# Optimization experiments

Measured on AMD Instinct MI355X. Metric: run time of the kernel, lower is better.

Reference implementation:

```python
import jax, jax.numpy as jnp
import numpy as np

B, S, D, DV = 1, 4096, 1024, 1024  # S == 4*D required by the data-dependent scale broadcast


def setup_inputs() -> dict:
    key = jax.random.key(0)
    kq, kk, kv, ks, kp = jax.random.split(key, 5)
    return {
        "q": jax.random.normal(kq, (B, S, D), dtype=jnp.float32),
        "k": jax.random.normal(kk, (B, S, D), dtype=jnp.float32),
        "v": jax.random.normal(kv, (B, S, DV), dtype=jnp.float32),
        "scale_factor": jax.random.normal(ks, (1,), dtype=jnp.float32),  # overwritten in forward
        "dropout_p": jax.random.uniform(kp, (1,), dtype=jnp.float32),   # overwritten in forward
    }


def reference(q, k, v, scale_factor, dropout_p):
    b, s, d = q.shape
    step = s // 4
    # data-dependent per-column scale: 4 strided rows of q flattened -> (B, 4*D) == (B, S)
    scale = q[:, ::step].reshape(b, -1)            # (B, S)
    qk = jnp.einsum('bsd,btd->bst', q, k)           # (B, S, S)
    scaled_qk = qk * scale[:, None, :]              # torch broadcast (B,S)->(1,1,S) since B==1
    softmax_qk = jax.nn.softmax(scaled_qk, axis=-1)
    # dropout with tensor p is ill-defined in torch; identity (eval semantics)
    return jnp.einsum('bst,btv->bsv', softmax_qk, v)
```

## Files before the change

kernel.cpp:

```cpp
#include <hip/hip_runtime.h>
#include <hip/hip_bf16.h>

typedef __bf16 bf16x8 __attribute__((ext_vector_type(8)));
typedef __bf16 bf16x4 __attribute__((ext_vector_type(4)));
typedef float f32x4 __attribute__((ext_vector_type(4)));

#define S_LEN 4096
#define DDIM  1024

#define MFMA __builtin_amdgcn_mfma_f32_16x16x32_bf16

#define BAR() do { asm volatile("" ::: "memory"); __builtin_amdgcn_s_barrier(); asm volatile("" ::: "memory"); } while (0)
#define VM6() asm volatile("s_waitcnt vmcnt(6)" ::: "memory")
#define VM4() asm volatile("s_waitcnt vmcnt(4)" ::: "memory")
#define VM0() asm volatile("s_waitcnt vmcnt(0)" ::: "memory")

__device__ __forceinline__ void gl_lds16(const __bf16* g, __bf16* l)
{
    __builtin_amdgcn_global_load_lds(
        (const __attribute__((address_space(1))) void*)g,
        (__attribute__((address_space(3))) void*)l, 16, 0, 0);
}

__global__ void prep_hilo(const float* __restrict__ q, const float* __restrict__ kk,
                          __bf16* __restrict__ qh, __bf16* __restrict__ ql,
                          __bf16* __restrict__ kh, __bf16* __restrict__ kl,
                          float* __restrict__ scale)
{
    const int gid = blockIdx.x * blockDim.x + threadIdx.x;
    if (gid < S_LEN) scale[gid] = q[((size_t)(gid >> 10) << 20) + (gid & 1023)];

    const int n8 = (S_LEN * DDIM) / 8;
    for (int i = gid; i < n8; i += gridDim.x * blockDim.x) {
        float4 a = *(const float4*)(q + (size_t)i * 8);
        float4 b = *(const float4*)(q + (size_t)i * 8 + 4);
        float va[8] = {a.x, a.y, a.z, a.w, b.x, b.y, b.z, b.w};
        bf16x8 h, l;
#pragma unroll
        for (int j = 0; j < 8; ++j) {
            __bf16 hh = (__bf16)va[j];
            h[j] = hh;
            l[j] = (__bf16)(va[j] - (float)hh);
        }
        *(bf16x8*)(qh + (size_t)i * 8) = h;
        *(bf16x8*)(ql + (size_t)i * 8) = l;

        a = *(const float4*)(kk + (size_t)i * 8);
        b = *(const float4*)(kk + (size_t)i * 8 + 4);
        float vb[8] = {a.x, a.y, a.z, a.w, b.x, b.y, b.z, b.w};
#pragma unroll
        for (int j = 0; j < 8; ++j) {
            __bf16 hh = (__bf16)vb[j];
            h[j] = hh;
            l[j] = (__bf16)(vb[j] - (float)hh);
        }
        *(bf16x8*)(kh + (size_t)i * 8) = h;
        *(bf16x8*)(kl + (size_t)i * 8) = l;
    }
}

__global__ void prep_vt(const float* __restrict__ v, __bf16* __restrict__ vt)
{
    __shared__ float tile[32][33];
    const int t0 = blockIdx.x * 32;
    const int d0 = blockIdx.y * 32;
    const int tx = threadIdx.x & 31;
    const int ty = threadIdx.x >> 5;
#pragma unroll
    for (int i = 0; i < 32; i += 8)
        tile[ty + i][tx] = v[(size_t)(t0 + ty + i) * DDIM + d0 + tx];
    __syncthreads();
#pragma unroll
    for (int i = 0; i < 32; i += 8)
        vt[(size_t)(d0 + ty + i) * S_LEN + t0 + tx] = (__bf16)tile[tx][ty + i];
}

__device__ __forceinline__ const __bf16* selA(const __bf16* qh, const __bf16* ql, int ps)
{ return ps == 1 ? ql : qh; }
__device__ __forceinline__ const __bf16* selB(const __bf16* kh, const __bf16* kl, int ps)
{ return ps == 2 ? kl : kh; }

template<int BUF, int RG>
__device__ __forceinline__ void stageG1(__bf16 (&lds)[2][4][8192], const __bf16* pl,
                                        int base, int koff, int w, int lane)
{
#pragma unroll
    for (int j = 0; j < 2; ++j) {
        const int ubase = (2 * w + j) * 64;
        const int u = ubase + lane;
        const int r = u >> 3, cu = u & 7;
        int grow;
        if (RG < 2) grow = base + ((r >> 6) << 7) + ((RG & 1) << 6) + (r & 63);
        else        grow = base + ((r >> 5) << 6) + ((RG & 1) << 5) + (r & 31);
        const __bf16* src = pl + (size_t)grow * DDIM + koff + ((cu ^ (r & 7)) << 3);
        gl_lds16(src, &lds[BUF][RG][0] + ubase * 8);
    }
}

template<int BUF, int MH>
__device__ __forceinline__ void rdA(bf16x8 (&a)[4][2], const __bf16 (&lds)[2][4][8192],
                                    int wr, int arow, int aoct)
{
#pragma unroll
    for (int mi = 0; mi < 4; ++mi)
#pragma unroll
        for (int ks = 0; ks < 2; ++ks) {
            const int lr = wr * 64 + mi * 16 + arow;
            const int cc = ks * 4 + aoct;
            a[mi][ks] = *(const bf16x8*)((const char*)&lds[BUF][MH][0]
                            + lr * 128 + ((cc ^ (lr & 7)) << 4));
        }
}

template<int BUF, int NH>
__device__ __forceinline__ void rdB(bf16x8 (&b)[2][2], const __bf16 (&lds)[2][4][8192],
                                    int wc, int arow, int aoct)
{
#pragma unroll
    for (int ni = 0; ni < 2; ++ni)
#pragma unroll
        for (int ks = 0; ks < 2; ++ks) {
            const int lr = wc * 32 + ni * 16 + arow;
            const int cc = ks * 4 + aoct;
            b[ni][ks] = *(const bf16x8*)((const char*)&lds[BUF][2 + NH][0]
                            + lr * 128 + ((cc ^ (lr & 7)) << 4));
        }
}

#define QMFMA(MH, NH, bb) \
    _Pragma("unroll") for (int ks = 0; ks < 2; ++ks) \
    _Pragma("unroll") for (int mi = 0; mi < 4; ++mi) \
    _Pragma("unroll") for (int ni = 0; ni < 2; ++ni) \
        acc[(MH)*4 + mi][(NH)*2 + ni] = MFMA(a[mi][ks], bb[ni][ks], acc[(MH)*4 + mi][(NH)*2 + ni], 0, 0, 0);

__global__ __launch_bounds__(512, 2) void gemm_qk(
    const __bf16* __restrict__ qh, const __bf16* __restrict__ ql,
    const __bf16* __restrict__ kh, const __bf16* __restrict__ kl,
    const float* __restrict__ scale, float* __restrict__ Sout)
{
    __shared__ __align__(16) __bf16 lds[2][4][8192];

    const int tid = threadIdx.x;
    const int w = tid >> 6, lane = tid & 63;
    const int arow = lane & 15, aoct = lane >> 4;
    const int wr = w >> 2, wc = w & 3;
    const int nb = (blockIdx.x & 7) * 32 + (blockIdx.x >> 3);
    const int m0 = (nb & 15) * 256, n0 = (nb >> 4) * 256;

    f32x4 acc[8][4];
#pragma unroll
    for (int i = 0; i < 8; ++i)
#pragma unroll
        for (int j = 0; j < 4; ++j) acc[i][j] = (f32x4){0.f, 0.f, 0.f, 0.f};

    stageG1<0, 0>(lds, selA(qh, ql, 0), m0, 0, w, lane);
    stageG1<0, 1>(lds, selA(qh, ql, 0), m0, 0, w, lane);
    stageG1<0, 2>(lds, selB(kh, kl, 0), n0, 0, w, lane);
    stageG1<0, 3>(lds, selB(kh, kl, 0), n0, 0, w, lane);
    stageG1<1, 0>(lds, selA(qh, ql, 0), m0, 64, w, lane);
    stageG1<1, 2>(lds, selB(kh, kl, 0), n0, 64, w, lane);
    stageG1<1, 3>(lds, selB(kh, kl, 0), n0, 64, w, lane);
    VM6(); BAR();

    for (int it = 0; it < 24; ++it) {
        const int t0 = 2 * it, t1 = 2 * it + 1;
        const bool last = (it == 23);
        const int ps1 = t1 >> 4, ko1 = (t1 & 15) << 6;
        const int ps2 = (t0 + 2) >> 4, ko2 = ((t0 + 2) & 15) << 6;
        const int ps3 = (t1 + 2) >> 4, ko3 = ((t1 + 2) & 15) << 6;
        bf16x8 a[4][2], b0[2][2], b1[2][2];

        rdA<0, 0>(a, lds, wr, arow, aoct);
        rdB<0, 0>(b0, lds, wc, arow, aoct);
        stageG1<1, 1>(lds, selA(qh, ql, ps1), m0, ko1, w, lane);
        BAR();
        __builtin_amdgcn_s_setprio(1); QMFMA(0, 0, b0); __builtin_amdgcn_s_setprio(0);
        BAR();
        rdB<0, 1>(b1, lds, wc, arow, aoct);
        if (!last) stageG1<0, 0>(lds, selA(qh, ql, ps2), m0, ko2, w, lane);
        BAR();
        __builtin_amdgcn_s_setprio(1); QMFMA(0, 1, b1); __builtin_amdgcn_s_setprio(0);
        BAR();
        rdA<0, 1>(a, lds, wr, arow, aoct);
        if (!last) stageG1<0, 2>(lds, selB(kh, kl, ps2), n0, ko2, w, lane);
        BAR();
        __builtin_amdgcn_s_setprio(1); QMFMA(1, 0, b0); __builtin_amdgcn_s_setprio(0);
        BAR();
        if (!last) stageG1<0, 3>(lds, selB(kh, kl, ps2), n0, ko2, w, lane);
        if (last) { VM0(); } else { VM6(); }
        BAR();
        __builtin_amdgcn_s_setprio(1); QMFMA(1, 1, b1); __builtin_amdgcn_s_setprio(0);
        BAR();
        rdA<1, 0>(a, lds, wr, arow, aoct);
        rdB<1, 0>(b0, lds, wc, arow, aoct);
        if (!last) stageG1<0, 1>(lds, selA(qh, ql, ps2), m0, ko2, w, lane);
        BAR();
        __builtin_amdgcn_s_setprio(1); QMFMA(0, 0, b0); __builtin_amdgcn_s_setprio(0);
        BAR();
        rdB<1, 1>(b1, lds, wc, arow, aoct);
        if (!last) stageG1<1, 0>(lds, selA(qh, ql, ps3), m0, ko3, w, lane);
        BAR();
        __builtin_amdgcn_s_setprio(1); QMFMA(0, 1, b1); __builtin_amdgcn_s_setprio(0);
        BAR();
        rdA<1, 1>(a, lds, wr, arow, aoct);
        if (!last) stageG1<1, 2>(lds, selB(kh, kl, ps3), n0, ko3, w, lane);
        BAR();
        __builtin_amdgcn_s_setprio(1); QMFMA(1, 0, b0); __builtin_amdgcn_s_setprio(0);
        BAR();
        if (!last) stageG1<1, 3>(lds, selB(kh, kl, ps3), n0, ko3, w, lane);
        if (last) { VM0(); } else { VM6(); }
        BAR();
        __builtin_amdgcn_s_setprio(1); QMFMA(1, 1, b1); __builtin_amdgcn_s_setprio(0);
        BAR();
    }

    const int nbase = n0 + wc * 64;
    float sc[4];
#pragma unroll
    for (int ni = 0; ni < 4; ++ni) sc[ni] = scale[nbase + ni * 16 + arow];
#pragma unroll
    for (int mi = 0; mi < 8; ++mi)
#pragma unroll
        for (int ni = 0; ni < 4; ++ni)
#pragma unroll
            for (int ii = 0; ii < 4; ++ii) {
                const int m = m0 + wr * 128 + mi * 16 + aoct * 4 + ii;
                Sout[(size_t)m * S_LEN + nbase + ni * 16 + arow] = acc[mi][ni][ii] * sc[ni];
            }
}

__global__ __launch_bounds__(256) void softmax_kernel(const float* __restrict__ S,
                                                      __bf16* __restrict__ P)
{
    __shared__ float red[8];
    const int row = blockIdx.x, tid = threadIdx.x;
    const int w = tid >> 6, lane = tid & 63;
    const float* sr = S + (size_t)row * S_LEN;
    float4 v[4];
#pragma unroll
    for (int c = 0; c < 4; ++c) v[c] = *(const float4*)(sr + c * 1024 + tid * 4);
    float mx = -3e38f;
#pragma unroll
    for (int c = 0; c < 4; ++c)
        mx = fmaxf(mx, fmaxf(fmaxf(v[c].x, v[c].y), fmaxf(v[c].z, v[c].w)));
#pragma unroll
    for (int sh = 32; sh >= 1; sh >>= 1) mx = fmaxf(mx, __shfl_xor(mx, sh));
    if (lane == 0) red[w] = mx;
    __syncthreads();
    mx = fmaxf(fmaxf(red[0], red[1]), fmaxf(red[2], red[3]));

    float e[4][4];
    float sum = 0.f;
#pragma unroll
    for (int c = 0; c < 4; ++c) {
        e[c][0] = __expf(v[c].x - mx); e[c][1] = __expf(v[c].y - mx);
        e[c][2] = __expf(v[c].z - mx); e[c][3] = __expf(v[c].w - mx);
        sum += (e[c][0] + e[c][1]) + (e[c][2] + e[c][3]);
    }
#pragma unroll
    for (int sh = 32; sh >= 1; sh >>= 1) sum += __shfl_xor(sum, sh);
    if (lane == 0) red[4 + w] = sum;
    __syncthreads();
    sum = (red[4] + red[5]) + (red[6] + red[7]);
    const float inv = 1.f / sum;
#pragma unroll
    for (int c = 0; c < 4; ++c) {
        bf16x4 o = {(__bf16)(e[c][0] * inv), (__bf16)(e[c][1] * inv),
                    (__bf16)(e[c][2] * inv), (__bf16)(e[c][3] * inv)};
        *(bf16x4*)(P + (size_t)row * 8192 + c * 1024 + tid * 4) = o;
    }
}

__device__ __forceinline__ void stagePV(__bf16* __restrict__ dst,
                                        const __bf16* __restrict__ P,
                                        const __bf16* __restrict__ vt,
                                        int m0, int n0, int t, int w, int lane)
{
#pragma unroll
    for (int j = 0; j < 2; ++j) {
        const int ubase = (2 * w + j) * 64;
        const int u = ubase + lane;
        const int r = u >> 3, cu = u & 7;
        const int kc = t * 64 + ((cu ^ (r & 7)) << 3);
        gl_lds16(P + (size_t)(m0 + r) * 8192 + kc, dst + ubase * 8);
        gl_lds16(vt + (size_t)(n0 + r) * S_LEN + kc, dst + 8192 + ubase * 8);
    }
}

__global__ __launch_bounds__(512, 1) void gemm_pv(const __bf16* __restrict__ P,
                                                  const __bf16* __restrict__ vt,
                                                  float* __restrict__ out)
{
    __shared__ __align__(16) __bf16 lds[3][2][8192];

    const int tid = threadIdx.x;
    const int w = tid >> 6, lane = tid & 63;
    const int arow = lane & 15, aoct = lane >> 4;
    const int wr = w >> 2, wc = w & 3;
    const int nb = (blockIdx.x & 7) * 32 + (blockIdx.x >> 3);
    const int m0 = (nb & 31) * 128, n0 = (nb >> 5) * 128;

    f32x4 acc[4][2];
#pragma unroll
    for (int i = 0; i < 4; ++i)
#pragma unroll
        for (int j = 0; j < 2; ++j) acc[i][j] = (f32x4){0.f, 0.f, 0.f, 0.f};

    stagePV(&lds[0][0][0], P, vt, m0, n0, 0, w, lane);
    stagePV(&lds[1][0][0], P, vt, m0, n0, 1, w, lane);
    VM4(); BAR();

    int c0 = 0, c1 = 1, c2 = 2;
    for (int t = 0; t < 64; ++t) {
        const char* pa = (const char*)&lds[c0][0][0];
        const char* pb = (const char*)&lds[c0][1][0];
        bf16x8 a[4][2], b[2][2];
#pragma unroll
        for (int mi = 0; mi < 4; ++mi)
#pragma unroll
            for (int ks = 0; ks < 2; ++ks) {
                const int lr = wr * 64 + mi * 16 + arow;
                const int cc = ks * 4 + aoct;
                a[mi][ks] = *(const bf16x8*)(pa + lr * 128 + ((cc ^ (lr & 7)) << 4));
            }
#pragma unroll
        for (int ni = 0; ni < 2; ++ni)
#pragma unroll
            for (int ks = 0; ks < 2; ++ks) {
                const int lr = wc * 32 + ni * 16 + arow;
                const int cc = ks * 4 + aoct;
                b[ni][ks] = *(const bf16x8*)(pb + lr * 128 + ((cc ^ (lr & 7)) << 4));
            }
        if (t < 62) stagePV(&lds[c2][0][0], P, vt, m0, n0, t + 2, w, lane);
        BAR();
        __builtin_amdgcn_s_setprio(1);
#pragma unroll
        for (int ks = 0; ks < 2; ++ks)
#pragma unroll
            for (int mi = 0; mi < 4; ++mi)
#pragma unroll
                for (int ni = 0; ni < 2; ++ni)
                    acc[mi][ni] = MFMA(a[mi][ks], b[ni][ks], acc[mi][ni], 0, 0, 0);
        __builtin_amdgcn_s_setprio(0);
        __builtin_amdgcn_sched_barrier(0);
        if (t <= 60) { VM4(); } else { VM0(); }
        BAR();
        const int tmp = c0; c0 = c1; c1 = c2; c2 = tmp;
    }

#pragma unroll
    for (int mi = 0; mi < 4; ++mi)
#pragma unroll
        for (int ni = 0; ni < 2; ++ni)
#pragma unroll
            for (int ii = 0; ii < 4; ++ii) {
                const int m = m0 + wr * 64 + mi * 16 + aoct * 4 + ii;
                const int n = n0 + wc * 32 + ni * 16 + arow;
                out[(size_t)m * DDIM + n] = acc[mi][ni][ii];
            }
}

extern "C" void kernel_launch(void* const* d_in, const int* in_sizes, int n_in,
                              void* d_out, int out_size, void* d_ws, size_t ws_size,
                              hipStream_t stream)
{
    const float* q = (const float*)d_in[0];
    const float* k = (const float*)d_in[1];
    const float* v = (const float*)d_in[2];
    float* out = (float*)d_out;

    const size_t PLANE = (size_t)S_LEN * DDIM * sizeof(__bf16);
    const size_t SOFF  = 5 * PLANE + 64 * 1024;
    const size_t NEEDED = SOFF + (size_t)S_LEN * S_LEN * sizeof(float);
    if (ws_size < NEEDED) return;

    char* ws = (char*)d_ws;
    __bf16* qh = (__bf16*)(ws);
    __bf16* ql = (__bf16*)(ws + PLANE);
    __bf16* kh = (__bf16*)(ws + 2 * PLANE);
    __bf16* kl = (__bf16*)(ws + 3 * PLANE);
    __bf16* vt = (__bf16*)(ws + 4 * PLANE);
    float* scale = (float*)(ws + 5 * PLANE);
    float* Smat = (float*)(ws + SOFF);
    __bf16* P = (__bf16*)Smat;

    prep_hilo<<<dim3(1024), dim3(256), 0, stream>>>(q, k, qh, ql, kh, kl, scale);
    prep_vt<<<dim3(S_LEN / 32, DDIM / 32), dim3(256), 0, stream>>>(v, vt);
    gemm_qk<<<dim3(256), dim3(512), 0, stream>>>(qh, ql, kh, kl, scale, Smat);
    softmax_kernel<<<dim3(S_LEN), dim3(256), 0, stream>>>(Smat, P);
    gemm_pv<<<dim3(256), dim3(512), 0, stream>>>(P, vt, out);
}
```

Baseline: 164.6 us.

## Fuse softmax into QK epilogue stats and PV prologue exponentiation

Removes the standalone softmax kernel. The QK GEMM epilogue now computes per-tile row max and sum-of-exp partials, and a small kernel combines them into a global max and inverse sum. The PV GEMM then loads fp32 scores directly, exponentiates them into bf16 in LDS and normalises the output at the end. This saves one full pass over the S matrix and the P write, but PV now streams fp32 scores through registers and recomputes the exponentials for each column block.

```diff
diff --git a/kernel.cpp b/kernel.cpp
--- a/kernel.cpp
+++ b/kernel.cpp
@@ -13,7 +13,9 @@
 #define BAR() do { asm volatile("" ::: "memory"); __builtin_amdgcn_s_barrier(); asm volatile("" ::: "memory"); } while (0)
 #define VM6() asm volatile("s_waitcnt vmcnt(6)" ::: "memory")
 #define VM4() asm volatile("s_waitcnt vmcnt(4)" ::: "memory")
+#define VM2() asm volatile("s_waitcnt vmcnt(2)" ::: "memory")
 #define VM0() asm volatile("s_waitcnt vmcnt(0)" ::: "memory")
+#define LGKM0() asm volatile("s_waitcnt lgkmcnt(0)" ::: "memory")
 
 __device__ __forceinline__ void gl_lds16(const __bf16* g, __bf16* l)
 {
@@ -136,7 +138,8 @@
 __global__ __launch_bounds__(512, 2) void gemm_qk(
     const __bf16* __restrict__ qh, const __bf16* __restrict__ ql,
     const __bf16* __restrict__ kh, const __bf16* __restrict__ kl,
-    const float* __restrict__ scale, float* __restrict__ Sout)
+    const float* __restrict__ scale, float* __restrict__ Sout,
+    float2* __restrict__ part)
 {
     __shared__ __align__(16) __bf16 lds[2][4][8192];
 
@@ -218,80 +221,71 @@
     float sc[4];
 #pragma unroll
     for (int ni = 0; ni < 4; ++ni) sc[ni] = scale[nbase + ni * 16 + arow];
-#pragma unroll
-    for (int mi = 0; mi < 8; ++mi)
+
+    float2* sst = (float2*)&lds[0][0][0];
+    __syncthreads();
+
+#pragma unroll
+    for (int mi = 0; mi < 8; ++mi) {
+#pragma unroll
+        for (int ni = 0; ni < 4; ++ni)
+#pragma unroll
+            for (int ii = 0; ii < 4; ++ii)
+                acc[mi][ni][ii] *= sc[ni];
+#pragma unroll
+        for (int ii = 0; ii < 4; ++ii) {
+            float m = fmaxf(fmaxf(acc[mi][0][ii], acc[mi][1][ii]),
+                            fmaxf(acc[mi][2][ii], acc[mi][3][ii]));
+#pragma unroll
+            for (int sh = 8; sh >= 1; sh >>= 1) m = fmaxf(m, __shfl_xor(m, sh));
+            float s = 0.f;
+#pragma unroll
+            for (int ni = 0; ni < 4; ++ni) s += __expf(acc[mi][ni][ii] - m);
+#pragma unroll
+            for (int sh = 8; sh >= 1; sh >>= 1) s += __shfl_xor(s, sh);
+            if (arow == 0)
+                sst[(wr * 128 + mi * 16 + aoct * 4 + ii) * 4 + wc] = make_float2(m, s);
+        }
 #pragma unroll
         for (int ni = 0; ni < 4; ++ni)
 #pragma unroll
             for (int ii = 0; ii < 4; ++ii) {
                 const int m = m0 + wr * 128 + mi * 16 + aoct * 4 + ii;
-                Sout[(size_t)m * S_LEN + nbase + ni * 16 + arow] = acc[mi][ni][ii] * sc[ni];
+                Sout[(size_t)m * S_LEN + nbase + ni * 16 + arow] = acc[mi][ni][ii];
             }
-}
-
-__global__ __launch_bounds__(256) void softmax_kernel(const float* __restrict__ S,
-                                                      __bf16* __restrict__ P)
-{
-    __shared__ float red[8];
-    const int row = blockIdx.x, tid = threadIdx.x;
-    const int w = tid >> 6, lane = tid & 63;
-    const float* sr = S + (size_t)row * S_LEN;
-    float4 v[4];
-#pragma unroll
-    for (int c = 0; c < 4; ++c) v[c] = *(const float4*)(sr + c * 1024 + tid * 4);
-    float mx = -3e38f;
-#pragma unroll
-    for (int c = 0; c < 4; ++c)
-        mx = fmaxf(mx, fmaxf(fmaxf(v[c].x, v[c].y), fmaxf(v[c].z, v[c].w)));
-#pragma unroll
-    for (int sh = 32; sh >= 1; sh >>= 1) mx = fmaxf(mx, __shfl_xor(mx, sh));
-    if (lane == 0) red[w] = mx;
+    }
     __syncthreads();
-    mx = fmaxf(fmaxf(red[0], red[1]), fmaxf(red[2], red[3]));
-
-    float e[4][4];
-    float sum = 0.f;
-#pragma unroll
-    for (int c = 0; c < 4; ++c) {
-        e[c][0] = __expf(v[c].x - mx); e[c][1] = __expf(v[c].y - mx);
-        e[c][2] = __expf(v[c].z - mx); e[c][3] = __expf(v[c].w - mx);
-        sum += (e[c][0] + e[c][1]) + (e[c][2] + e[c][3]);
-    }
-#pragma unroll
-    for (int sh = 32; sh >= 1; sh >>= 1) sum += __shfl_xor(sum, sh);
-    if (lane == 0) red[4 + w] = sum;
-    __syncthreads();
-    sum = (red[4] + red[5]) + (red[6] + red[7]);
-    const float inv = 1.f / sum;
-#pragma unroll
-    for (int c = 0; c < 4; ++c) {
-        bf16x4 o = {(__bf16)(e[c][0] * inv), (__bf16)(e[c][1] * inv),
-                    (__bf16)(e[c][2] * inv), (__bf16)(e[c][3] * inv)};
-        *(bf16x4*)(P + (size_t)row * 8192 + c * 1024 + tid * 4) = o;
-    }
-}
-
-__device__ __forceinline__ void stagePV(__bf16* __restrict__ dst,
-                                        const __bf16* __restrict__ P,
-                                        const __bf16* __restrict__ vt,
-                                        int m0, int n0, int t, int w, int lane)
-{
-#pragma unroll
-    for (int j = 0; j < 2; ++j) {
-        const int ubase = (2 * w + j) * 64;
-        const int u = ubase + lane;
-        const int r = u >> 3, cu = u & 7;
-        const int kc = t * 64 + ((cu ^ (r & 7)) << 3);
-        gl_lds16(P + (size_t)(m0 + r) * 8192 + kc, dst + ubase * 8);
-        gl_lds16(vt + (size_t)(n0 + r) * S_LEN + kc, dst + 8192 + ubase * 8);
-    }
-}
-
-__global__ __launch_bounds__(512, 1) void gemm_pv(const __bf16* __restrict__ P,
+    if (tid < 256) {
+        float2 s0 = sst[tid * 4 + 0], s1 = sst[tid * 4 + 1];
+        float2 s2 = sst[tid * 4 + 2], s3 = sst[tid * 4 + 3];
+        float M = fmaxf(fmaxf(s0.x, s1.x), fmaxf(s2.x, s3.x));
+        float L = s0.y * __expf(s0.x - M) + s1.y * __expf(s1.x - M)
+                + s2.y * __expf(s2.x - M) + s3.y * __expf(s3.x - M);
+        part[(size_t)(n0 >> 8) * S_LEN + m0 + tid] = make_float2(M, L);
+    }
+}
+
+__global__ void combine_stats(const float2* __restrict__ part, float2* __restrict__ fin)
+{
+    const int r = blockIdx.x * 256 + threadIdx.x;
+    float M = -3e38f;
+#pragma unroll
+    for (int t = 0; t < 16; ++t) M = fmaxf(M, part[(size_t)t * S_LEN + r].x);
+    float L = 0.f;
+#pragma unroll
+    for (int t = 0; t < 16; ++t) {
+        float2 p = part[(size_t)t * S_LEN + r];
+        L += p.y * __expf(p.x - M);
+    }
+    fin[r] = make_float2(M, 1.f / L);
+}
+
+__global__ __launch_bounds__(512, 1) void gemm_pv(const float* __restrict__ S,
                                                   const __bf16* __restrict__ vt,
+                                                  const float2* __restrict__ fin,
                                                   float* __restrict__ out)
 {
-    __shared__ __align__(16) __bf16 lds[3][2][8192];
+    __shared__ __align__(16) __bf16 lds[2][2][8192];
 
     const int tid = threadIdx.x;
     const int w = tid >> 6, lane = tid & 63;
@@ -300,20 +294,55 @@
     const int nb = (blockIdx.x & 7) * 32 + (blockIdx.x >> 3);
     const int m0 = (nb & 31) * 128, n0 = (nb >> 5) * 128;
 
+    int rr[2], kof[2];
+    float Mrow[2];
+#pragma unroll
+    for (int j = 0; j < 2; ++j) {
+        const int u = (2 * w + j) * 64 + lane;
+        rr[j] = u >> 3;
+        kof[j] = ((u & 7) ^ (rr[j] & 7)) * 8;
+        Mrow[j] = fin[m0 + rr[j]].x;
+    }
+
     f32x4 acc[4][2];
 #pragma unroll
     for (int i = 0; i < 4; ++i)
 #pragma unroll
         for (int j = 0; j < 2; ++j) acc[i][j] = (f32x4){0.f, 0.f, 0.f, 0.f};
 
-    stagePV(&lds[0][0][0], P, vt, m0, n0, 0, w, lane);
-    stagePV(&lds[1][0][0], P, vt, m0, n0, 1, w, lane);
-    VM4(); BAR();
-
-    int c0 = 0, c1 = 1, c2 = 2;
+    float4 ar[2][2];
+    bf16x8 pb[2];
+
+#define LOADA(t) do { _Pragma("unroll") for (int j = 0; j < 2; ++j) { \
+        const float* p_ = S + (size_t)(m0 + rr[j]) * S_LEN + (t) * 64 + kof[j]; \
+        ar[j][0] = *(const float4*)p_; ar[j][1] = *(const float4*)(p_ + 4); } } while (0)
+#define TRANS() do { _Pragma("unroll") for (int j = 0; j < 2; ++j) { \
+        pb[j][0] = (__bf16)__expf(ar[j][0].x - Mrow[j]); \
+        pb[j][1] = (__bf16)__expf(ar[j][0].y - Mrow[j]); \
+        pb[j][2] = (__bf16)__expf(ar[j][0].z - Mrow[j]); \
+        pb[j][3] = (__bf16)__expf(ar[j][0].w - Mrow[j]); \
+        pb[j][4] = (__bf16)__expf(ar[j][1].x - Mrow[j]); \
+        pb[j][5] = (__bf16)__expf(ar[j][1].y - Mrow[j]); \
+        pb[j][6] = (__bf16)__expf(ar[j][1].z - Mrow[j]); \
+        pb[j][7] = (__bf16)__expf(ar[j][1].w - Mrow[j]); } } while (0)
+#define WRITEA(buf) do { _Pragma("unroll") for (int j = 0; j < 2; ++j) \
+        *(bf16x8*)(&lds[buf][0][0] + ((2 * w + j) * 64 + lane) * 8) = pb[j]; } while (0)
+#define STAGEV(buf, t) do { _Pragma("unroll") for (int j = 0; j < 2; ++j) { \
+        const int ub_ = (2 * w + j) * 64; \
+        gl_lds16(vt + (size_t)(n0 + rr[j]) * S_LEN + (t) * 64 + kof[j], \
+                 &lds[buf][1][0] + ub_ * 8); } } while (0)
+
+    LOADA(0); STAGEV(0, 0);
+    VM0();
+    TRANS(); WRITEA(0);
+    LOADA(1);
+    LGKM0(); BAR();
+    STAGEV(1, 1);
+
     for (int t = 0; t < 64; ++t) {
-        const char* pa = (const char*)&lds[c0][0][0];
-        const char* pb = (const char*)&lds[c0][1][0];
+        const int cur = t & 1, nxt = cur ^ 1;
+        const char* pa = (const char*)&lds[cur][0][0];
+        const char* pbv = (const char*)&lds[cur][1][0];
         bf16x8 a[4][2], b[2][2];
 #pragma unroll
         for (int mi = 0; mi < 4; ++mi)
@@ -329,10 +358,12 @@
             for (int ks = 0; ks < 2; ++ks) {
                 const int lr = wc * 32 + ni * 16 + arow;
                 const int cc = ks * 4 + aoct;
-                b[ni][ks] = *(const bf16x8*)(pb + lr * 128 + ((cc ^ (lr & 7)) << 4));
+                b[ni][ks] = *(const bf16x8*)(pbv + lr * 128 + ((cc ^ (lr & 7)) << 4));
             }
-        if (t < 62) stagePV(&lds[c2][0][0], P, vt, m0, n0, t + 2, w, lane);
-        BAR();
+        if (t < 63) { VM2(); TRANS(); }
+        BAR();
+        if (t < 63) WRITEA(nxt);
+        if (t < 62) LOADA(t + 2);
         __builtin_amdgcn_s_setprio(1);
 #pragma unroll
         for (int ks = 0; ks < 2; ++ks)
@@ -343,21 +374,28 @@
                     acc[mi][ni] = MFMA(a[mi][ks], b[ni][ks], acc[mi][ni], 0, 0, 0);
         __builtin_amdgcn_s_setprio(0);
         __builtin_amdgcn_sched_barrier(0);
-        if (t <= 60) { VM4(); } else { VM0(); }
-        BAR();
-        const int tmp = c0; c0 = c1; c1 = c2; c2 = tmp;
+        LGKM0();
+        if (t < 62) { VM4(); } else { VM0(); }
+        BAR();
+        if (t < 62) STAGEV(cur, t + 2);
     }
 
 #pragma unroll
     for (int mi = 0; mi < 4; ++mi)
 #pragma unroll
-        for (int ni = 0; ni < 2; ++ni)
-#pragma unroll
-            for (int ii = 0; ii < 4; ++ii) {
-                const int m = m0 + wr * 64 + mi * 16 + aoct * 4 + ii;
+        for (int ii = 0; ii < 4; ++ii) {
+            const int m = m0 + wr * 64 + mi * 16 + aoct * 4 + ii;
+            const float invl = fin[m].y;
+#pragma unroll
+            for (int ni = 0; ni < 2; ++ni) {
                 const int n = n0 + wc * 32 + ni * 16 + arow;
-                out[(size_t)m * DDIM + n] = acc[mi][ni][ii];
+                out[(size_t)m * DDIM + n] = acc[mi][ni][ii] * invl;
             }
+        }
+#undef LOADA
+#undef TRANS
+#undef WRITEA
+#undef STAGEV
 }
 
 extern "C" void kernel_launch(void* const* d_in, const int* in_sizes, int n_in,
@@ -371,7 +409,10 @@
 
     const size_t PLANE = (size_t)S_LEN * DDIM * sizeof(__bf16);
     const size_t SOFF  = 5 * PLANE + 64 * 1024;
-    const size_t NEEDED = SOFF + (size_t)S_LEN * S_LEN * sizeof(float);
+    const size_t SBYTES = (size_t)S_LEN * S_LEN * sizeof(float);
+    const size_t POFF  = SOFF + SBYTES;
+    const size_t FOFF  = POFF + 16 * (size_t)S_LEN * sizeof(float2);
+    const size_t NEEDED = FOFF + (size_t)S_LEN * sizeof(float2);
     if (ws_size < NEEDED) return;
 
     char* ws = (char*)d_ws;
@@ -382,11 +423,12 @@
     __bf16* vt = (__bf16*)(ws + 4 * PLANE);
     float* scale = (float*)(ws + 5 * PLANE);
     float* Smat = (float*)(ws + SOFF);
-    __bf16* P = (__bf16*)Smat;
+    float2* part = (float2*)(ws + POFF);
+    float2* fin = (float2*)(ws + FOFF);
 
     prep_hilo<<<dim3(1024), dim3(256), 0, stream>>>(q, k, qh, ql, kh, kl, scale);
     prep_vt<<<dim3(S_LEN / 32, DDIM / 32), dim3(256), 0, stream>>>(v, vt);
-    gemm_qk<<<dim3(256), dim3(512), 0, stream>>>(qh, ql, kh, kl, scale, Smat);
-    softmax_kernel<<<dim3(S_LEN), dim3(256), 0, stream>>>(Smat, P);
-    gemm_pv<<<dim3(256), dim3(512), 0, stream>>>(P, vt, out);
-}
+    gemm_qk<<<dim3(256), dim3(512), 0, stream>>>(qh, ql, kh, kl, scale, Smat, part);
+    combine_stats<<<dim3(S_LEN / 256), dim3(256), 0, stream>>>(part, fin);
+    gemm_pv<<<dim3(256), dim3(512), 0, stream>>>(Smat, vt, fin, out);
+}
```

After: 200.9 us. 22.1% more time.
